# Kernel optimization log

Measured on AMD Instinct MI355X. Metric: run time of the kernel, lower is better.

Reference implementation:

```python
import jax, jax.numpy as jnp
import numpy as np

B, V, T, R = 128, 128000, 4096, 64
REP_PENALTY = 1.2   # _rep_penalty (set_repetition_penalty)
MAX_REPS = 3        # _max_reps
REQUIRED_BOOST = 5.0  # _required_boost


def setup_inputs() -> dict:
    key = jax.random.key(0)
    k1, k2, k3, k4 = jax.random.split(key, 4)
    logits = jax.random.normal(k1, (B, V), dtype=jnp.float32)
    generated_so_far = jax.random.randint(k2, (B, T), 0, V, dtype=jnp.int32)
    forbidden_mask = jax.random.bernoulli(k3, 0.01, (V,))
    required_tokens = jax.random.randint(k4, (R,), 0, V, dtype=jnp.int32)
    return {"logits": logits, "generated_so_far": generated_so_far,
            "forbidden_mask": forbidden_mask, "required_tokens": required_tokens}


def reference(logits, generated_so_far, forbidden_mask, required_tokens):
    Bn, Vn = logits.shape
    neg_inf = jnp.float32(-jnp.inf)

    # 1) forbidden tokens -> -inf
    out = jnp.where(forbidden_mask[None, :], neg_inf, logits)

    # per-row token occurrence counts (vectorized bincount) [B, V]
    counts = jnp.zeros((Bn, Vn), jnp.int32).at[
        jnp.arange(Bn)[:, None], generated_so_far
    ].add(1)

    # 2) boost required tokens not yet generated and not forbidden
    present = counts[:, required_tokens] > 0              # [B, R]
    allowed = ~forbidden_mask[required_tokens]            # [R]
    boost = jnp.where((~present) & allowed[None, :],
                      jnp.float32(REQUIRED_BOOST), jnp.float32(0.0))
    out = out.at[:, required_tokens].add(boost)

    # 3) repetition penalty on tokens with count >= MAX_REPS (skip -inf)
    penalized = jnp.where(out > 0, out / REP_PENALTY, out * REP_PENALTY)
    out = jnp.where((counts >= MAX_REPS) & (out != neg_inf), penalized, out)
    return out
```

## Files before the change

kernel.cpp:

```cpp
#include <hip/hip_runtime.h>
#include <cstdint>
#include <cstddef>

#define BB 128
#define VV 128000
#define TT 4096
#define SS 16
#define VR (VV / SS)
#define HW2 (VR / 4)
#define NT 256

typedef float vf4 __attribute__((ext_vector_type(4)));


__device__ __forceinline__ int block_detect(const unsigned char* maskb,
                                            unsigned* det, int tid) {
  if (tid == 0) *det = 0u;
  __syncthreads();
  const uint4* md = (const uint4*)maskb;
  unsigned a = 0u, c = 0u;
#pragma unroll
  for (int k = 0; k < 4; ++k) {
    uint4 w = md[tid + k * NT];
    unsigned o = w.x | w.y | w.z | w.w;
    a |= o & 0x000000FFu;
    c |= o & 0xFFFFFF00u;
  }
  unsigned long long ba = __ballot(a != 0u);
  unsigned long long bc = __ballot(c != 0u);
  if ((tid & 63) == 0) {
    unsigned bits = (ba ? 1u : 0u) | (bc ? 2u : 0u);
    if (bits) atomicOr(det, bits);
  }
  __syncthreads();
  return (*det == 3u) ? 1 : 3;
}

template<int ML>
__global__ __launch_bounds__(NT) void enforce_kernel(
    const float* __restrict__ logits,
    const int*  __restrict__ gen,
    const unsigned char* __restrict__ maskb,
    const int*  __restrict__ req,
    float* __restrict__ out,
    int R)
{
  __shared__ unsigned hist[HW2];
  __shared__ int cand[64];
  __shared__ unsigned ncand;
  const int tid = threadIdx.x;

  const int L    = blockIdx.x;
  const int xcd  = L & 7;
  const int q    = L >> 3;
  const int s    = q & (SS - 1);
  const int b    = (q >> 4) * 8 + xcd;
  const int vbase = s * VR;

  int ml = ML;
  if constexpr (ML == -1) {
    __shared__ unsigned det;
    ml = block_detect(maskb, &det, tid);
  }

  for (int i = tid; i < HW2; i += NT) hist[i] = 0u;
  if (tid == 0) ncand = 0u;
  __syncthreads();

  const float SENT = __uint_as_float(0xFF7F0000u);
  const float RINV = 1.0f / 1.2f;

  auto forb1 = [&](int t) -> bool {
    if (ml == 1) return maskb[t] != 0;
    return ((const int*)maskb)[t] != 0;
  };

  const vf4* lrow = (const vf4*)(logits + (size_t)b * VV + vbase);
  vf4*       orow = (vf4*)(out + (size_t)b * VV + vbase);
  const unsigned* m8  = (const unsigned*)(maskb + vbase);
  const int4*     m32 = (const int4*)((const int*)maskb + vbase);

  auto load_mask = [&](int i) -> unsigned {
    if (ml == 1) return m8[i];
    int4 m = m32[i];
    return (m.x ? 1u : 0u) | (m.y ? 0x100u : 0u) |
           (m.z ? 0x10000u : 0u) | (m.w ? 0x1000000u : 0u);
  };

  for (int i0 = tid; i0 < HW2; i0 += 2 * NT) {
    const int i1 = i0 + NT;
    const bool p1 = (i1 < HW2);
    vf4 x0 = lrow[i0];
    unsigned f0 = load_mask(i0);
    vf4 x1 = {0.f, 0.f, 0.f, 0.f};
    unsigned f1 = 0u;
    if (p1) { x1 = lrow[i1]; f1 = load_mask(i1); }

    vf4 r0, r1;
#pragma unroll
    for (int j = 0; j < 4; ++j)
      r0[j] = ((f0 >> (j * 8)) & 0xFFu) ? SENT : x0[j];
    orow[i0] = r0;
    if (p1) {
#pragma unroll
      for (int j = 0; j < 4; ++j)
        r1[j] = ((f1 >> (j * 8)) & 0xFFu) ? SENT : x1[j];
      orow[i1] = r1;
    }
  }

  const int4* grow = (const int4*)(gen + b * TT);
  for (int i = tid; i < TT / 4; i += NT) {
    int4 g = grow[i];
    const int t4[4] = {g.x, g.y, g.z, g.w};
#pragma unroll
    for (int j = 0; j < 4; ++j) {
      const int t = t4[j];
      unsigned d = (unsigned)(t - vbase);
      if (d < (unsigned)VR) {
        const unsigned sh = (d & 3u) * 8u;
        unsigned old = atomicAdd(&hist[d >> 2], 1u << sh);
        if (((old >> sh) & 0xFFu) == 2u) {
          unsigned k = atomicAdd(&ncand, 1u);
          if (k < 64u) cand[k] = t;
        }
      }
    }
  }
  __syncthreads();

  const unsigned nc = ncand < 64u ? ncand : 64u;
  for (unsigned k = tid; k < nc; k += NT) {
    const int t = cand[k];
    if (!forb1(t)) {
      float* p = out + (size_t)b * VV + t;
      float v = *p;
      *p = (v > 0.0f) ? v * RINV : v * 1.2f;
    }
  }

  for (int r = tid; r < R; r += NT) {
    const int t = req[r];
    unsigned d = (unsigned)(t - vbase);
    if (d < (unsigned)VR) {
      unsigned cnt = (hist[d >> 2] >> ((d & 3u) * 8u)) & 0xFFu;
      if (cnt == 0u && !forb1(t))
        atomicAdd(out + (size_t)b * VV + t, 5.0f);
    }
  }
}

extern "C" void kernel_launch(void* const* d_in, const int* in_sizes, int n_in,
                              void* d_out, int out_size, void* d_ws, size_t ws_size,
                              hipStream_t stream) {
  const float* logits = (const float*)d_in[0];
  const int*   gen    = (const int*)d_in[1];
  const unsigned char* maskb = (const unsigned char*)d_in[2];
  const int*   req    = (const int*)d_in[3];
  float* out = (float*)d_out;

  int R = in_sizes[3];
  if (R >= 256 && (R & 3) == 0) R >>= 2;

  int ml;
  if (in_sizes[0] == BB * VV * 4) {
    ml = (in_sizes[2] == VV) ? 1 : 3;
  } else {
    ml = -1;
  }

  const int G = BB * SS;
  if (ml == 1)      enforce_kernel<1><<<G, NT, 0, stream>>>(logits, gen, maskb, req, out, R);
  else if (ml == 3) enforce_kernel<3><<<G, NT, 0, stream>>>(logits, gen, maskb, req, out, R);
  else              enforce_kernel<-1><<<G, NT, 0, stream>>>(logits, gen, maskb, req, out, R);
}
```

Measured before the change: 123.9 us.

## Split streaming copy and histogram into separate blocks with workspace exception patching

Each vocabulary window now gets two blocks. One streams the masked copy of logits to the output, unrolled four ways. The other builds the shared-memory histogram, computes the penalised and boosted values straight from logits, and writes them as exception records into a workspace. A second small kernel then scatters those records into the output. This runs the bandwidth-bound copy alongside the atomic-heavy histogram instead of one after the other within a block, at the cost of an extra launch, workspace traffic, and a cap on exceptions per window.

```diff
diff --git a/kernel.cpp b/kernel.cpp
--- a/kernel.cpp
+++ b/kernel.cpp
@@ -5,13 +5,20 @@
 #define BB 128
 #define VV 128000
 #define TT 4096
-#define SS 16
-#define VR (VV / SS)
-#define HW2 (VR / 4)
+#define NWIN 2048
+#define WVR (VV / 16)
+#define WHW (WVR / 4)
 #define NT 256
+#define EXC_CAP 96
 
 typedef float vf4 __attribute__((ext_vector_type(4)));
 
+
+__device__ __forceinline__ void win_decode(int id, int& b, int& vbase) {
+  const int xcd = id & 7, q = id >> 3, s = q & 15;
+  b = (q >> 4) * 8 + xcd;
+  vbase = s * WVR;
+}
 
 __device__ __forceinline__ int block_detect(const unsigned char* maskb,
                                             unsigned* det, int tid) {
@@ -37,7 +44,149 @@
 }
 
 template<int ML>
-__global__ __launch_bounds__(NT) void enforce_kernel(
+__global__ __launch_bounds__(NT) void enforce_fused(
+    const float* __restrict__ logits,
+    const int*  __restrict__ gen,
+    const unsigned char* __restrict__ maskb,
+    const int*  __restrict__ req,
+    float* __restrict__ out,
+    unsigned* __restrict__ wsc,
+    uint2*    __restrict__ wse,
+    int R)
+{
+  __shared__ unsigned hist[WHW];
+  __shared__ uint2 exc[EXC_CAP];
+  __shared__ unsigned nexc;
+  const int tid = threadIdx.x;
+  const int L   = blockIdx.x;
+  const int id  = L >> 1;
+  int b, vbase; win_decode(id, b, vbase);
+
+  int ml = ML;
+  if constexpr (ML == -1) {
+    __shared__ unsigned det;
+    ml = block_detect(maskb, &det, tid);
+  }
+
+  const float SENT = __uint_as_float(0xFF7F0000u);
+  const float RINV = 1.0f / 1.2f;
+  auto forb1 = [&](int t) -> bool {
+    if (ml == 1) return maskb[t] != 0;
+    return ((const int*)maskb)[t] != 0;
+  };
+
+  if ((L & 1) == 0) {
+    const vf4* lrow = (const vf4*)(logits + (size_t)b * VV + vbase);
+    vf4*       orow = (vf4*)(out + (size_t)b * VV + vbase);
+    const unsigned* m8  = (const unsigned*)(maskb + vbase);
+    const int4*     m32 = (const int4*)((const int*)maskb + vbase);
+    auto lmask = [&](int i) -> unsigned {
+      if (ml == 1) return m8[i];
+      int4 m = m32[i];
+      return (m.x ? 1u : 0u) | (m.y ? 0x100u : 0u) |
+             (m.z ? 0x10000u : 0u) | (m.w ? 0x1000000u : 0u);
+    };
+    for (int i0 = tid; i0 < WHW; i0 += 4 * NT) {
+      const int i1 = i0 + NT, i2 = i0 + 2 * NT, i3 = i0 + 3 * NT;
+      const bool p1 = i1 < WHW, p2 = i2 < WHW, p3 = i3 < WHW;
+      vf4 x0 = lrow[i0];           unsigned f0 = lmask(i0);
+      vf4 x1 = {0,0,0,0}, x2 = {0,0,0,0}, x3 = {0,0,0,0};
+      unsigned f1 = 0, f2 = 0, f3 = 0;
+      if (p1) { x1 = lrow[i1]; f1 = lmask(i1); }
+      if (p2) { x2 = lrow[i2]; f2 = lmask(i2); }
+      if (p3) { x3 = lrow[i3]; f3 = lmask(i3); }
+      vf4 r0, r1, r2, r3;
+#pragma unroll
+      for (int j = 0; j < 4; ++j) r0[j] = ((f0 >> (j*8)) & 0xFFu) ? SENT : x0[j];
+      orow[i0] = r0;
+      if (p1) {
+#pragma unroll
+        for (int j = 0; j < 4; ++j) r1[j] = ((f1 >> (j*8)) & 0xFFu) ? SENT : x1[j];
+        orow[i1] = r1;
+      }
+      if (p2) {
+#pragma unroll
+        for (int j = 0; j < 4; ++j) r2[j] = ((f2 >> (j*8)) & 0xFFu) ? SENT : x2[j];
+        orow[i2] = r2;
+      }
+      if (p3) {
+#pragma unroll
+        for (int j = 0; j < 4; ++j) r3[j] = ((f3 >> (j*8)) & 0xFFu) ? SENT : x3[j];
+        orow[i3] = r3;
+      }
+    }
+  } else {
+    for (int i = tid; i < WHW; i += NT) hist[i] = 0u;
+    if (tid == 0) nexc = 0u;
+    __syncthreads();
+
+    const int4* grow = (const int4*)(gen + b * TT);
+    for (int i = tid; i < TT / 4; i += NT) {
+      int4 g = grow[i];
+      const int t4[4] = {g.x, g.y, g.z, g.w};
+#pragma unroll
+      for (int j = 0; j < 4; ++j) {
+        const int t = t4[j];
+        unsigned d = (unsigned)(t - vbase);
+        if (d < (unsigned)WVR) {
+          const unsigned sh = (d & 3u) * 8u;
+          unsigned old = atomicAdd(&hist[d >> 2], 1u << sh);
+          if (((old >> sh) & 0xFFu) == 2u && !forb1(t)) {
+            float v  = logits[(size_t)b * VV + t];
+            float pv = (v > 0.0f) ? v * RINV : v * 1.2f;
+            unsigned k = atomicAdd(&nexc, 1u);
+            if (k < EXC_CAP) exc[k] = make_uint2(d, __float_as_uint(pv));
+          }
+        }
+      }
+    }
+    __syncthreads();
+
+    for (int r = tid; r < R; r += NT) {
+      const int t = req[r];
+      unsigned d = (unsigned)(t - vbase);
+      if (d < (unsigned)WVR) {
+        bool first = true; int mult = 0;
+        for (int j = 0; j < R; ++j) {
+          if (req[j] == t) { if (j < r) first = false; ++mult; }
+        }
+        if (first) {
+          unsigned cnt = (hist[d >> 2] >> ((d & 3u) * 8u)) & 0xFFu;
+          if (cnt == 0u && !forb1(t)) {
+            float v = logits[(size_t)b * VV + t] + 5.0f * (float)mult;
+            unsigned k = atomicAdd(&nexc, 1u);
+            if (k < EXC_CAP) exc[k] = make_uint2(d, __float_as_uint(v));
+          }
+        }
+      }
+    }
+    __syncthreads();
+
+    unsigned n = nexc < EXC_CAP ? nexc : EXC_CAP;
+    if (tid == 0) wsc[id] = n;
+    for (unsigned k = tid; k < n; k += NT)
+      wse[(size_t)id * EXC_CAP + k] = exc[k];
+  }
+}
+
+__global__ __launch_bounds__(NT) void apply_exc(
+    float* __restrict__ out,
+    const unsigned* __restrict__ wsc,
+    const uint2* __restrict__ wse)
+{
+  const int w = blockIdx.x * NT + threadIdx.x;
+  if (w >= NWIN) return;
+  int b, vbase; win_decode(w, b, vbase);
+  unsigned n = wsc[w]; if (n > EXC_CAP) n = EXC_CAP;
+  const uint2* e = wse + (size_t)w * EXC_CAP;
+  for (unsigned k = 0; k < n; ++k) {
+    uint2 q = e[k];
+    out[(size_t)b * VV + vbase + q.x] = __uint_as_float(q.y);
+  }
+}
+
+template<int ML>
+__global__ __launch_bounds__(NT) void enforce_mono(
     const float* __restrict__ logits,
     const int*  __restrict__ gen,
     const unsigned char* __restrict__ maskb,
@@ -45,70 +194,53 @@
     float* __restrict__ out,
     int R)
 {
-  __shared__ unsigned hist[HW2];
+  __shared__ unsigned hist[WHW];
   __shared__ int cand[64];
   __shared__ unsigned ncand;
   const int tid = threadIdx.x;
-
-  const int L    = blockIdx.x;
-  const int xcd  = L & 7;
-  const int q    = L >> 3;
-  const int s    = q & (SS - 1);
-  const int b    = (q >> 4) * 8 + xcd;
-  const int vbase = s * VR;
+  int b, vbase; win_decode(blockIdx.x, b, vbase);
 
   int ml = ML;
   if constexpr (ML == -1) {
     __shared__ unsigned det;
     ml = block_detect(maskb, &det, tid);
   }
-
-  for (int i = tid; i < HW2; i += NT) hist[i] = 0u;
+  for (int i = tid; i < WHW; i += NT) hist[i] = 0u;
   if (tid == 0) ncand = 0u;
   __syncthreads();
 
   const float SENT = __uint_as_float(0xFF7F0000u);
   const float RINV = 1.0f / 1.2f;
-
   auto forb1 = [&](int t) -> bool {
     if (ml == 1) return maskb[t] != 0;
     return ((const int*)maskb)[t] != 0;
   };
-
   const vf4* lrow = (const vf4*)(logits + (size_t)b * VV + vbase);
   vf4*       orow = (vf4*)(out + (size_t)b * VV + vbase);
   const unsigned* m8  = (const unsigned*)(maskb + vbase);
   const int4*     m32 = (const int4*)((const int*)maskb + vbase);
-
-  auto load_mask = [&](int i) -> unsigned {
+  auto lmask = [&](int i) -> unsigned {
     if (ml == 1) return m8[i];
     int4 m = m32[i];
     return (m.x ? 1u : 0u) | (m.y ? 0x100u : 0u) |
            (m.z ? 0x10000u : 0u) | (m.w ? 0x1000000u : 0u);
   };
-
-  for (int i0 = tid; i0 < HW2; i0 += 2 * NT) {
+  for (int i0 = tid; i0 < WHW; i0 += 2 * NT) {
     const int i1 = i0 + NT;
-    const bool p1 = (i1 < HW2);
-    vf4 x0 = lrow[i0];
-    unsigned f0 = load_mask(i0);
-    vf4 x1 = {0.f, 0.f, 0.f, 0.f};
-    unsigned f1 = 0u;
-    if (p1) { x1 = lrow[i1]; f1 = load_mask(i1); }
-
+    const bool p1 = (i1 < WHW);
+    vf4 x0 = lrow[i0]; unsigned f0 = lmask(i0);
+    vf4 x1 = {0,0,0,0}; unsigned f1 = 0u;
+    if (p1) { x1 = lrow[i1]; f1 = lmask(i1); }
     vf4 r0, r1;
 #pragma unroll
-    for (int j = 0; j < 4; ++j)
-      r0[j] = ((f0 >> (j * 8)) & 0xFFu) ? SENT : x0[j];
+    for (int j = 0; j < 4; ++j) r0[j] = ((f0 >> (j*8)) & 0xFFu) ? SENT : x0[j];
     orow[i0] = r0;
     if (p1) {
 #pragma unroll
-      for (int j = 0; j < 4; ++j)
-        r1[j] = ((f1 >> (j * 8)) & 0xFFu) ? SENT : x1[j];
+      for (int j = 0; j < 4; ++j) r1[j] = ((f1 >> (j*8)) & 0xFFu) ? SENT : x1[j];
       orow[i1] = r1;
     }
   }
-
   const int4* grow = (const int4*)(gen + b * TT);
   for (int i = tid; i < TT / 4; i += NT) {
     int4 g = grow[i];
@@ -117,7 +249,7 @@
     for (int j = 0; j < 4; ++j) {
       const int t = t4[j];
       unsigned d = (unsigned)(t - vbase);
-      if (d < (unsigned)VR) {
+      if (d < (unsigned)WVR) {
         const unsigned sh = (d & 3u) * 8u;
         unsigned old = atomicAdd(&hist[d >> 2], 1u << sh);
         if (((old >> sh) & 0xFFu) == 2u) {
@@ -128,21 +260,18 @@
     }
   }
   __syncthreads();
-
   const unsigned nc = ncand < 64u ? ncand : 64u;
   for (unsigned k = tid; k < nc; k += NT) {
     const int t = cand[k];
     if (!forb1(t)) {
-      float* p = out + (size_t)b * VV + t;
-      float v = *p;
-      *p = (v > 0.0f) ? v * RINV : v * 1.2f;
-    }
-  }
-
+      float v = logits[(size_t)b * VV + t];
+      out[(size_t)b * VV + t] = (v > 0.0f) ? v * RINV : v * 1.2f;
+    }
+  }
   for (int r = tid; r < R; r += NT) {
     const int t = req[r];
     unsigned d = (unsigned)(t - vbase);
-    if (d < (unsigned)VR) {
+    if (d < (unsigned)WVR) {
       unsigned cnt = (hist[d >> 2] >> ((d & 3u) * 8u)) & 0xFFu;
       if (cnt == 0u && !forb1(t))
         atomicAdd(out + (size_t)b * VV + t, 5.0f);
@@ -169,8 +298,20 @@
     ml = -1;
   }
 
-  const int G = BB * SS;
-  if (ml == 1)      enforce_kernel<1><<<G, NT, 0, stream>>>(logits, gen, maskb, req, out, R);
-  else if (ml == 3) enforce_kernel<3><<<G, NT, 0, stream>>>(logits, gen, maskb, req, out, R);
-  else              enforce_kernel<-1><<<G, NT, 0, stream>>>(logits, gen, maskb, req, out, R);
-}
+  const size_t NEED = 8192 + (size_t)NWIN * EXC_CAP * sizeof(uint2);
+  if (d_ws != nullptr && ws_size >= NEED) {
+    unsigned* wsc = (unsigned*)d_ws;
+    uint2*    wse = (uint2*)((char*)d_ws + 8192);
+    if (ml == 1)
+      enforce_fused<1><<<2 * NWIN, NT, 0, stream>>>(logits, gen, maskb, req, out, wsc, wse, R);
+    else if (ml == 3)
+      enforce_fused<3><<<2 * NWIN, NT, 0, stream>>>(logits, gen, maskb, req, out, wsc, wse, R);
+    else
+      enforce_fused<-1><<<2 * NWIN, NT, 0, stream>>>(logits, gen, maskb, req, out, wsc, wse, R);
+    apply_exc<<<(NWIN + NT - 1) / NT, NT, 0, stream>>>(out, wsc, wse);
+  } else {
+    if (ml == 1)      enforce_mono<1><<<NWIN, NT, 0, stream>>>(logits, gen, maskb, req, out, R);
+    else if (ml == 3) enforce_mono<3><<<NWIN, NT, 0, stream>>>(logits, gen, maskb, req, out, R);
+    else              enforce_mono<-1><<<NWIN, NT, 0, stream>>>(logits, gen, maskb, req, out, R);
+  }
+}
```

Result: slower. 145.0 us (+17.0%).
